# Kernel optimization log

Measured on AMD Instinct MI355X. Metric: run time of the kernel, lower is better.

## Reference

```python
import jax, jax.numpy as jnp
import numpy as np


def _hardswish(x):
    # torch.nn.Hardswish: x * relu6(x + 3) / 6
    return x * jnp.clip(x + 3.0, 0.0, 6.0) * (1.0 / 6.0)


def _local_linear(x, W, b):
    # x: [B, N, G*ig], W: [G, og, ig], b: [G, og]
    # Faithful to torch Local_Linear: split -> per-group Linear -> unsqueeze(-1)
    # -> cat on last dim -> flatten(2). The cat/flatten interleaves groups:
    # out[..., o*G + g] = y[..., g, o].
    B, N, C = x.shape
    G, og, ig = W.shape
    xg = x.reshape(B, N, G, ig)
    y = jnp.einsum('bngi,goi->bngo', xg, W) + b  # [B, N, G, og]
    return jnp.transpose(y, (0, 1, 3, 2)).reshape(B, N, og * G)


def setup_inputs() -> dict:
    key = jax.random.key(0)
    ks = jax.random.split(key, 5)
    B, N, C = 8, 2048, 1152
    G = 9
    hid = 4608
    ig1, og1 = C // G, hid // G      # 128, 512
    ig2, og2 = hid // G, C // G      # 512, 128
    x = jax.random.normal(ks[0], (B, N, C), dtype=jnp.float32)
    W1 = jax.random.normal(ks[1], (G, og1, ig1), dtype=jnp.float32) * (1.0 / np.sqrt(ig1))
    b1 = jax.random.normal(ks[2], (G, og1), dtype=jnp.float32) * 0.01
    W2 = jax.random.normal(ks[3], (G, og2, ig2), dtype=jnp.float32) * (1.0 / np.sqrt(ig2))
    b2 = jax.random.normal(ks[4], (G, og2), dtype=jnp.float32) * 0.01
    return {"x": x, "W1": W1, "b1": b1, "W2": W2, "b2": b2}


def reference(x, W1, b1, W2, b2):
    h = _local_linear(x, W1, b1)   # [B, N, 4608] (interleaved group layout)
    h = _hardswish(h)
    out = _local_linear(h, W2, b2)  # [B, N, 1152]
    return out
```

## Files before the change

kernel.cpp:

```cpp
#include <hip/hip_runtime.h>

typedef short bf16x8 __attribute__((ext_vector_type(8)));
typedef float f32x4 __attribute__((ext_vector_type(4)));

#define NG   9
#define CIN  1152
#define IG1  128
#define OG1  512
#define IG2  512
#define OG2  128
#define KP   576
#define MT   32
#define MTOT 16384

__device__ __forceinline__ short f2bf(float f) {
    unsigned u = __float_as_uint(f);
    u += 0x7fff + ((u >> 16) & 1);
    return (short)(u >> 16);
}

__global__ __launch_bounds__(256) void prep_w1(const float* __restrict__ w1, short* __restrict__ w1b) {
    int i = blockIdx.x * 256 + threadIdx.x;
    if (i < NG * OG1 * IG1) w1b[i] = f2bf(w1[i]);
}

__global__ __launch_bounds__(256) void prep_w2(const float* __restrict__ w2, short* __restrict__ w2p) {
    int i = blockIdx.x * 256 + threadIdx.x;
    if (i >= NG * OG2 * KP) return;
    int g2  = i / (OG2 * KP);
    int rem = i - g2 * (OG2 * KP);
    int o2  = rem / KP;
    int kp  = rem - o2 * KP;
    int g1 = kp >> 6, r = kp & 63;
    int olo = (512 * g2 - g1 + 8) / 9;
    int j = 9 * (olo + r) + g1 - 512 * g2;
    float v = (j < 512) ? w2[(g2 * OG2 + o2) * IG2 + j] : 0.0f;
    w2p[i] = f2bf(v);
}

__global__ __launch_bounds__(512) void fused(const float* __restrict__ x,
                                             const short* __restrict__ w1b, const float* __restrict__ b1,
                                             const short* __restrict__ w2p, const float* __restrict__ b2,
                                             float* __restrict__ out) {
    __shared__ __attribute__((aligned(16))) char smem[110592];
    short* xs = (short*)smem;
    short* ht = (short*)(smem + 73728);
    float* outs = (float*)smem;

    const int t = threadIdx.x;
    const int m0 = blockIdx.x * MT;
    const int w = t >> 6, lane = t & 63, lr = lane & 15, lg = lane >> 4;

    {
        int2 z = {0, 0};
#pragma unroll
        for (int i = 0; i < 9; ++i) *(int2*)(ht + (i * 512 + t) * 4) = z;
    }
#pragma unroll
    for (int i = 0; i < 9; ++i) {
        int f = i * 512 + t;
        int row = f / 144, c8 = f - row * 144;
        const float* gp = x + (size_t)(m0 + row) * CIN + c8 * 8;
        float4 v0 = *(const float4*)gp;
        float4 v1 = *(const float4*)(gp + 4);
        bf16x8 s;
        s[0]=f2bf(v0.x); s[1]=f2bf(v0.y); s[2]=f2bf(v0.z); s[3]=f2bf(v0.w);
        s[4]=f2bf(v1.x); s[5]=f2bf(v1.y); s[6]=f2bf(v1.z); s[7]=f2bf(v1.w);
        *(bf16x8*)(xs + (row * 144 + (c8 ^ (row & 7))) * 8) = s;
    }

    f32x4 acc2[2][8];
    f32x4 acc2b[2];
#pragma unroll
    for (int mi = 0; mi < 2; ++mi) {
#pragma unroll
        for (int ni = 0; ni < 8; ++ni) acc2[mi][ni] = (f32x4){0.f,0.f,0.f,0.f};
        acc2b[mi] = (f32x4){0.f,0.f,0.f,0.f};
    }
    __syncthreads();

    for (int g1 = 0; g1 < NG; ++g1) {
        f32x4 acc1[4][2];
#pragma unroll
        for (int oi = 0; oi < 4; ++oi)
#pragma unroll
            for (int mi = 0; mi < 2; ++mi) acc1[oi][mi] = (f32x4){0.f,0.f,0.f,0.f};
#pragma unroll
        for (int kf = 0; kf < 4; ++kf) {
            bf16x8 bx[2];
#pragma unroll
            for (int mi = 0; mi < 2; ++mi) {
                int row = mi * 16 + lr;
                bx[mi] = *(const bf16x8*)(xs + (row * 144 + ((g1 * 16 + kf * 4 + lg) ^ (row & 7))) * 8);
            }
#pragma unroll
            for (int oi = 0; oi < 4; ++oi) {
                bf16x8 af = *(const bf16x8*)(w1b + ((size_t)(g1 * OG1 + w * 64 + oi * 16 + lr) * IG1 + kf * 32 + lg * 8));
#pragma unroll
                for (int mi = 0; mi < 2; ++mi)
                    acc1[oi][mi] = __builtin_amdgcn_mfma_f32_16x16x32_bf16(af, bx[mi], acc1[oi][mi], 0, 0, 0);
            }
        }
        __syncthreads();
#pragma unroll
        for (int oi = 0; oi < 4; ++oi) {
            int ob = w * 64 + oi * 16 + lg * 4;
            float4 bias = *(const float4*)(b1 + g1 * OG1 + ob);
#pragma unroll
            for (int q = 0; q < 4; ++q) {
                int o  = ob + q;
                int c  = 9 * o + g1;
                int g2 = c >> 9;
                int olo = (512 * g2 - g1 + 8) / 9;
                int hc = g2 * 64 + (o - olo);
#pragma unroll
                for (int mi = 0; mi < 2; ++mi) {
                    int m = mi * 16 + lr;
                    float v = acc1[oi][mi][q] + ((const float*)&bias)[q];
                    v = v * fminf(fmaxf(v + 3.0f, 0.0f), 6.0f) * (1.0f / 6.0f);
                    *(short*)((char*)ht + m * 1152 + (((hc >> 3) ^ (m & 7)) << 4) + (hc & 7) * 2) = f2bf(v);
                }
            }
        }
        __syncthreads();
#pragma unroll
        for (int kf = 0; kf < 2; ++kf) {
            bf16x8 a_[2], a8_[2];
#pragma unroll
            for (int mi = 0; mi < 2; ++mi) {
                int m = mi * 16 + lr;
                a_[mi]  = *(const bf16x8*)((char*)ht + m * 1152 + (((w * 8 + kf * 4 + lg) ^ (m & 7)) << 4));
                a8_[mi] = *(const bf16x8*)((char*)ht + m * 1152 + (((64 + kf * 4 + lg) ^ (m & 7)) << 4));
            }
#pragma unroll
            for (int ni = 0; ni < 8; ++ni) {
                bf16x8 bfr = *(const bf16x8*)(w2p + (size_t)(w * 128 + ni * 16 + lr) * KP + g1 * 64 + kf * 32 + lg * 8);
#pragma unroll
                for (int mi = 0; mi < 2; ++mi)
                    acc2[mi][ni] = __builtin_amdgcn_mfma_f32_16x16x32_bf16(a_[mi], bfr, acc2[mi][ni], 0, 0, 0);
            }
            bf16x8 b8 = *(const bf16x8*)(w2p + (size_t)(8 * 128 + w * 16 + lr) * KP + g1 * 64 + kf * 32 + lg * 8);
#pragma unroll
            for (int mi = 0; mi < 2; ++mi)
                acc2b[mi] = __builtin_amdgcn_mfma_f32_16x16x32_bf16(a8_[mi], b8, acc2b[mi], 0, 0, 0);
        }
    }

#pragma unroll
    for (int h = 0; h < 2; ++h) {
        __syncthreads();
#pragma unroll
        for (int ni = 0; ni < 8; ++ni) {
            float bias = b2[w * OG2 + ni * 16 + lr];
            int c = (ni * 16 + lr) * 9 + w;
#pragma unroll
            for (int q = 0; q < 4; ++q)
                outs[(lg * 4 + q) * 1156 + c] = acc2[h][ni][q] + bias;
        }
        {
            float bias8 = b2[8 * OG2 + w * 16 + lr];
            int c8 = (w * 16 + lr) * 9 + 8;
#pragma unroll
            for (int q = 0; q < 4; ++q)
                outs[(lg * 4 + q) * 1156 + c8] = acc2b[h][q] + bias8;
        }
        __syncthreads();
#pragma unroll
        for (int i = 0; i < 9; ++i) {
            int f4 = i * 512 + t;
            int row = f4 / 288, c4 = f4 - row * 288;
            float4 v = *(const float4*)&outs[row * 1156 + c4 * 4];
            *(float4*)&out[(size_t)(m0 + h * 16 + row) * CIN + c4 * 4] = v;
        }
    }
}

extern "C" void kernel_launch(void* const* d_in, const int* in_sizes, int n_in,
                              void* d_out, int out_size, void* d_ws, size_t ws_size,
                              hipStream_t stream) {
    const float* x  = (const float*)d_in[0];
    const float* w1 = (const float*)d_in[1];
    const float* b1 = (const float*)d_in[2];
    const float* w2 = (const float*)d_in[3];
    const float* b2 = (const float*)d_in[4];
    float* out = (float*)d_out;

    short* w1b = (short*)d_ws;
    short* w2p = (short*)((char*)d_ws + (size_t)NG * OG1 * IG1 * 2);

    prep_w1<<<(NG * OG1 * IG1 + 255) / 256, 256, 0, stream>>>(w1, w1b);
    prep_w2<<<(NG * OG2 * KP + 255) / 256, 256, 0, stream>>>(w2, w2p);
    fused<<<MTOT / MT, 512, 0, stream>>>(x, w1b, b1, w2p, b2, out);
}
```

Measured before the change: 228.3 us.

## Stream x from global, double-buffer hidden tile, shrink LDS, merge prep kernels

The kernel no longer stages the whole bf16 x tile in LDS. Each wave now loads its x fragments straight from global memory and converts them per group, and the hidden-activation tile is double-buffered by group parity. This removes one barrier per group and cuts LDS from about 108KB to about 72KB, so more blocks can be resident per CU (launch bounds now ask for 4). The two weight-prep kernels are also merged into one launch. The cost is redundant global reads of x across waves and conversions inside the main loop, plus extra register pressure from the occupancy hint.

```diff
diff --git a/kernel.cpp b/kernel.cpp
--- a/kernel.cpp
+++ b/kernel.cpp
@@ -1,4 +1,5 @@
 #include <hip/hip_runtime.h>
+#include <hip/hip_bf16.h>
 
 typedef short bf16x8 __attribute__((ext_vector_type(8)));
 typedef float f32x4 __attribute__((ext_vector_type(4)));
@@ -12,39 +13,42 @@
 #define KP   576
 #define MT   32
 #define MTOT 16384
+#define HTB  36864
+#define OSTRIDE 1156
 
 __device__ __forceinline__ short f2bf(float f) {
     unsigned u = __float_as_uint(f);
     u += 0x7fff + ((u >> 16) & 1);
     return (short)(u >> 16);
 }
-
-__global__ __launch_bounds__(256) void prep_w1(const float* __restrict__ w1, short* __restrict__ w1b) {
-    int i = blockIdx.x * 256 + threadIdx.x;
-    if (i < NG * OG1 * IG1) w1b[i] = f2bf(w1[i]);
+__device__ __forceinline__ short cvt1(float f) {
+    __hip_bfloat16 h = __float2bfloat16(f);
+    return *reinterpret_cast<short*>(&h);
 }
 
-__global__ __launch_bounds__(256) void prep_w2(const float* __restrict__ w2, short* __restrict__ w2p) {
+__global__ __launch_bounds__(256) void prep(const float* __restrict__ w1, const float* __restrict__ w2,
+                                            short* __restrict__ w1b, short* __restrict__ w2p) {
     int i = blockIdx.x * 256 + threadIdx.x;
-    if (i >= NG * OG2 * KP) return;
-    int g2  = i / (OG2 * KP);
-    int rem = i - g2 * (OG2 * KP);
+    const int NW1 = NG * OG1 * IG1;
+    if (i < NW1) { w1b[i] = f2bf(w1[i]); return; }
+    int j = i - NW1;
+    if (j >= NG * OG2 * KP) return;
+    int g2  = j / (OG2 * KP);
+    int rem = j - g2 * (OG2 * KP);
     int o2  = rem / KP;
     int kp  = rem - o2 * KP;
     int g1 = kp >> 6, r = kp & 63;
     int olo = (512 * g2 - g1 + 8) / 9;
-    int j = 9 * (olo + r) + g1 - 512 * g2;
-    float v = (j < 512) ? w2[(g2 * OG2 + o2) * IG2 + j] : 0.0f;
-    w2p[i] = f2bf(v);
+    int jj = 9 * (olo + r) + g1 - 512 * g2;
+    float v = (jj < 512) ? w2[(g2 * OG2 + o2) * IG2 + jj] : 0.0f;
+    w2p[j] = f2bf(v);
 }
 
-__global__ __launch_bounds__(512) void fused(const float* __restrict__ x,
-                                             const short* __restrict__ w1b, const float* __restrict__ b1,
-                                             const short* __restrict__ w2p, const float* __restrict__ b2,
-                                             float* __restrict__ out) {
-    __shared__ __attribute__((aligned(16))) char smem[110592];
-    short* xs = (short*)smem;
-    short* ht = (short*)(smem + 73728);
+__global__ __launch_bounds__(512, 4) void fused(const float* __restrict__ x,
+                                                const short* __restrict__ w1b, const float* __restrict__ b1,
+                                                const short* __restrict__ w2p, const float* __restrict__ b2,
+                                                float* __restrict__ out) {
+    __shared__ __attribute__((aligned(16))) char smem[73984];
     float* outs = (float*)smem;
 
     const int t = threadIdx.x;
@@ -52,21 +56,9 @@
     const int w = t >> 6, lane = t & 63, lr = lane & 15, lg = lane >> 4;
 
     {
-        int2 z = {0, 0};
+        int4 z = {0, 0, 0, 0};
 #pragma unroll
-        for (int i = 0; i < 9; ++i) *(int2*)(ht + (i * 512 + t) * 4) = z;
-    }
-#pragma unroll
-    for (int i = 0; i < 9; ++i) {
-        int f = i * 512 + t;
-        int row = f / 144, c8 = f - row * 144;
-        const float* gp = x + (size_t)(m0 + row) * CIN + c8 * 8;
-        float4 v0 = *(const float4*)gp;
-        float4 v1 = *(const float4*)(gp + 4);
-        bf16x8 s;
-        s[0]=f2bf(v0.x); s[1]=f2bf(v0.y); s[2]=f2bf(v0.z); s[3]=f2bf(v0.w);
-        s[4]=f2bf(v1.x); s[5]=f2bf(v1.y); s[6]=f2bf(v1.z); s[7]=f2bf(v1.w);
-        *(bf16x8*)(xs + (row * 144 + (c8 ^ (row & 7))) * 8) = s;
+        for (int i = 0; i < 9; ++i) *(int4*)(smem + (i * 512 + t) * 16) = z;
     }
 
     f32x4 acc2[2][8];
@@ -80,6 +72,8 @@
     __syncthreads();
 
     for (int g1 = 0; g1 < NG; ++g1) {
+        char* htb = smem + (g1 & 1) * HTB;
+
         f32x4 acc1[4][2];
 #pragma unroll
         for (int oi = 0; oi < 4; ++oi)
@@ -90,8 +84,13 @@
             bf16x8 bx[2];
 #pragma unroll
             for (int mi = 0; mi < 2; ++mi) {
-                int row = mi * 16 + lr;
-                bx[mi] = *(const bf16x8*)(xs + (row * 144 + ((g1 * 16 + kf * 4 + lg) ^ (row & 7))) * 8);
+                const float* p = x + (size_t)(m0 + mi * 16 + lr) * CIN + g1 * IG1 + kf * 32 + lg * 8;
+                float4 v0 = *(const float4*)p;
+                float4 v1 = *(const float4*)(p + 4);
+                bf16x8 s;
+                s[0]=cvt1(v0.x); s[1]=cvt1(v0.y); s[2]=cvt1(v0.z); s[3]=cvt1(v0.w);
+                s[4]=cvt1(v1.x); s[5]=cvt1(v1.y); s[6]=cvt1(v1.z); s[7]=cvt1(v1.w);
+                bx[mi] = s;
             }
 #pragma unroll
             for (int oi = 0; oi < 4; ++oi) {
@@ -101,7 +100,7 @@
                     acc1[oi][mi] = __builtin_amdgcn_mfma_f32_16x16x32_bf16(af, bx[mi], acc1[oi][mi], 0, 0, 0);
             }
         }
-        __syncthreads();
+
 #pragma unroll
         for (int oi = 0; oi < 4; ++oi) {
             int ob = w * 64 + oi * 16 + lg * 4;
@@ -118,19 +117,20 @@
                     int m = mi * 16 + lr;
                     float v = acc1[oi][mi][q] + ((const float*)&bias)[q];
                     v = v * fminf(fmaxf(v + 3.0f, 0.0f), 6.0f) * (1.0f / 6.0f);
-                    *(short*)((char*)ht + m * 1152 + (((hc >> 3) ^ (m & 7)) << 4) + (hc & 7) * 2) = f2bf(v);
+                    *(short*)(htb + m * 1152 + (((hc >> 3) ^ (m & 7)) << 4) + (hc & 7) * 2) = cvt1(v);
                 }
             }
         }
         __syncthreads();
+
 #pragma unroll
         for (int kf = 0; kf < 2; ++kf) {
             bf16x8 a_[2], a8_[2];
 #pragma unroll
             for (int mi = 0; mi < 2; ++mi) {
                 int m = mi * 16 + lr;
-                a_[mi]  = *(const bf16x8*)((char*)ht + m * 1152 + (((w * 8 + kf * 4 + lg) ^ (m & 7)) << 4));
-                a8_[mi] = *(const bf16x8*)((char*)ht + m * 1152 + (((64 + kf * 4 + lg) ^ (m & 7)) << 4));
+                a_[mi]  = *(const bf16x8*)(htb + m * 1152 + (((w * 8 + kf * 4 + lg) ^ (m & 7)) << 4));
+                a8_[mi] = *(const bf16x8*)(htb + m * 1152 + (((64 + kf * 4 + lg) ^ (m & 7)) << 4));
             }
 #pragma unroll
             for (int ni = 0; ni < 8; ++ni) {
@@ -155,21 +155,21 @@
             int c = (ni * 16 + lr) * 9 + w;
 #pragma unroll
             for (int q = 0; q < 4; ++q)
-                outs[(lg * 4 + q) * 1156 + c] = acc2[h][ni][q] + bias;
+                outs[(lg * 4 + q) * OSTRIDE + c] = acc2[h][ni][q] + bias;
         }
         {
             float bias8 = b2[8 * OG2 + w * 16 + lr];
             int c8 = (w * 16 + lr) * 9 + 8;
 #pragma unroll
             for (int q = 0; q < 4; ++q)
-                outs[(lg * 4 + q) * 1156 + c8] = acc2b[h][q] + bias8;
+                outs[(lg * 4 + q) * OSTRIDE + c8] = acc2b[h][q] + bias8;
         }
         __syncthreads();
 #pragma unroll
         for (int i = 0; i < 9; ++i) {
             int f4 = i * 512 + t;
             int row = f4 / 288, c4 = f4 - row * 288;
-            float4 v = *(const float4*)&outs[row * 1156 + c4 * 4];
+            float4 v = *(const float4*)&outs[row * OSTRIDE + c4 * 4];
             *(float4*)&out[(size_t)(m0 + h * 16 + row) * CIN + c4 * 4] = v;
         }
     }
@@ -188,7 +188,7 @@
     short* w1b = (short*)d_ws;
     short* w2p = (short*)((char*)d_ws + (size_t)NG * OG1 * IG1 * 2);
 
-    prep_w1<<<(NG * OG1 * IG1 + 255) / 256, 256, 0, stream>>>(w1, w1b);
-    prep_w2<<<(NG * OG2 * KP + 255) / 256, 256, 0, stream>>>(w2, w2p);
+    const int nprep = NG * OG1 * IG1 + NG * OG2 * KP;
+    prep<<<(nprep + 255) / 256, 256, 0, stream>>>(w1, w2, w1b, w2p);
     fused<<<MTOT / MT, 512, 0, stream>>>(x, w1b, b1, w2p, b2, out);
 }
```

Result: slower. 357.1 us (+56.4%).
